# Kernel tuning notes

Measured on AMD Instinct MI355X. Metric: run time of the kernel, lower is better.

The kernel has to match this reference:

```python
import jax, jax.numpy as jnp
import numpy as np
from jax import lax

B, T, U, H, V = 4, 256, 48, 512, 1024
BLANK = V - 1  # blank = vocab_size - 1, as in Transducer.__init__


def setup_inputs() -> dict:
    key = jax.random.key(0)
    k1, k2, k3, k4 = jax.random.split(key, 4)
    enc_state = jax.random.normal(k1, (B, T, H), jnp.float32)       # encoder output
    dec_state = jax.random.normal(k2, (B, U + 1, H), jnp.float32)   # decoder output (blank-prepended targets)
    W = jax.random.normal(k3, (V, H), jnp.float32) / np.sqrt(H)     # joint proj weight
    b = jnp.zeros((V,), jnp.float32)                                # joint proj bias
    targets = jax.random.randint(k4, (B, U), 0, V - 1).astype(jnp.int32)  # labels, never blank
    inputs_length = jnp.full((B,), T, jnp.int32)
    targets_length = jnp.full((B,), U, jnp.int32)
    return {"enc_state": enc_state, "dec_state": dec_state, "W": W, "b": b,
            "targets": targets, "inputs_length": inputs_length,
            "targets_length": targets_length}


def _rnnt_loss_single(log_probs, targets, t_len, u_len):
    # log_probs: (T, U+1, V); forward-variable alpha DP of RNNT loss.
    lp_blank = log_probs[:, :, BLANK]                                   # (T, U+1)
    lp_label = jnp.take_along_axis(log_probs[:, :-1, :],
                                   targets[None, :, None], axis=2)[..., 0]  # (T, U)
    # first row: only label emissions, alpha[0,u] = sum_{k<u} lp_label[0,k]
    row0 = jnp.concatenate([jnp.zeros((1,), log_probs.dtype),
                            jnp.cumsum(lp_label[0])])                   # (U+1,)

    def row_step(prev_row, t):
        # alpha[t,u] = logaddexp(alpha[t-1,u] + blank[t-1,u], alpha[t,u-1] + label[t,u-1])
        a = prev_row + lp_blank[t - 1]                                  # (U+1,) blank transitions

        def u_step(carry, xs):
            a_u, lab = xs
            cur = jnp.logaddexp(a_u, carry + lab)
            return cur, cur

        _, rest = lax.scan(u_step, a[0], (a[1:], lp_label[t]))
        row = jnp.concatenate([a[:1], rest])
        return row, row

    _, rows = lax.scan(row_step, row0, jnp.arange(1, T))
    alpha = jnp.concatenate([row0[None], rows], axis=0)                 # (T, U+1)
    # negative log-likelihood: final blank emission from (t_len-1, u_len)
    return -(alpha[t_len - 1, u_len] + lp_blank[t_len - 1, u_len])


def reference(enc_state, dec_state, W, b, targets, inputs_length, targets_length):
    # JointNet: broadcast-add (repeat in torch) then linear projection
    joint = enc_state[:, :, None, :] + dec_state[:, None, :, :]         # (B, T, U+1, H)
    logits = jnp.einsum('btuh,vh->btuv', joint, W) + b                  # (B, T, U+1, V)
    log_probs = jax.nn.log_softmax(logits, axis=-1)
    loss = jax.vmap(_rnnt_loss_single)(log_probs, targets, inputs_length, targets_length)
    return loss  # per-sample losses (reduction='None')
```

## Files before the change

### kernel.cpp

```cpp
#include <hip/hip_runtime.h>
#include <math.h>

#define B_ 4
#define T_ 256
#define U_ 48
#define H_ 512
#define V_ 1024
#define BLANK_ (V_-1)

#define GM 1220
#define GM_ENC 1024
#define APAD 1280

#define INVLN2 1.4426950408889634f
#define LN2F   0.6931471805599453f

typedef __attribute__((ext_vector_type(8))) short short8;
typedef __attribute__((ext_vector_type(4))) float f32x4;

__device__ __forceinline__ unsigned short f2bf(float x) {
    union { float f; unsigned int u; } c; c.f = x;
    unsigned int r = c.u + 0x7FFF + ((c.u >> 16) & 1);
    return (unsigned short)(r >> 16);
}
__device__ __forceinline__ float bf2f(unsigned short u) {
    union { unsigned int i; float f; } c; c.i = ((unsigned int)u) << 16; return c.f;
}
__device__ __forceinline__ unsigned int cvt_pk_bf16(float lo, float hi) {
    unsigned int r;
    asm("v_cvt_pk_bf16_f32 %0, %1, %2" : "=v"(r) : "v"(lo), "v"(hi));
    return r;
}
__device__ __forceinline__ int wave_shr1_i(int x, int fill) {
    return __builtin_amdgcn_update_dpp(fill, x, 0x138 , 0xf, 0xf, false);
}
__device__ __forceinline__ float wave_shr1_f(float x, float fill) {
    return __builtin_bit_cast(float,
        wave_shr1_i(__builtin_bit_cast(int, x), __builtin_bit_cast(int, fill)));
}
__device__ __forceinline__ double wave_shr1_d(double x, double fill) {
    unsigned long long xb = __builtin_bit_cast(unsigned long long, x);
    unsigned long long fb = __builtin_bit_cast(unsigned long long, fill);
    int lo = wave_shr1_i((int)(unsigned)xb, (int)(unsigned)fb);
    int hi = wave_shr1_i((int)(xb >> 32), (int)(fb >> 32));
    unsigned long long r = ((unsigned long long)(unsigned)hi << 32) | (unsigned)lo;
    return __builtin_bit_cast(double, r);
}

__global__ __launch_bounds__(512) void gemm1_kernel(
    const float* __restrict__ enc, const float* __restrict__ dec,
    const float* __restrict__ W, const float* __restrict__ bias,
    unsigned short* __restrict__ Pexp)
{
    __shared__ __attribute__((aligned(16))) unsigned short As[128 * 64];
    __shared__ __attribute__((aligned(16))) unsigned short Bs[128 * 64];
    const int tid  = threadIdx.x;
    const int lane = tid & 63, wave = tid >> 6;
    const int wm = wave >> 2, wn = wave & 3;
    const int row0 = blockIdx.y * 128, col0 = blockIdx.x * 128;
    const int srow = tid >> 2;
    const int scg  = (tid & 3) * 16;

    f32x4 acc[4][2];
    #pragma unroll
    for (int mi = 0; mi < 4; ++mi)
        #pragma unroll
        for (int ni = 0; ni < 2; ++ni)
            acc[mi][ni] = (f32x4){0.f, 0.f, 0.f, 0.f};

    float4 ra[4], rb[4];
    auto loadAB = [&](int k0) {
        float4 z = make_float4(0.f, 0.f, 0.f, 0.f);
        ra[0] = ra[1] = ra[2] = ra[3] = z;
        int gr = row0 + srow;
        if (gr < GM) {
            const float* s = (gr < GM_ENC)
                ? enc + (size_t)gr * H_ + k0 + scg
                : dec + (size_t)(gr - GM_ENC) * H_ + k0 + scg;
            ra[0] = *(const float4*)s;       ra[1] = *(const float4*)(s + 4);
            ra[2] = *(const float4*)(s + 8); ra[3] = *(const float4*)(s + 12);
        }
        const float* s = W + (size_t)(col0 + srow) * H_ + k0 + scg;
        rb[0] = *(const float4*)s;       rb[1] = *(const float4*)(s + 4);
        rb[2] = *(const float4*)(s + 8); rb[3] = *(const float4*)(s + 12);
    };
    auto stage = [&]() {
        uint4 w0 = { cvt_pk_bf16(ra[0].x, ra[0].y), cvt_pk_bf16(ra[0].z, ra[0].w),
                     cvt_pk_bf16(ra[1].x, ra[1].y), cvt_pk_bf16(ra[1].z, ra[1].w) };
        uint4 w1 = { cvt_pk_bf16(ra[2].x, ra[2].y), cvt_pk_bf16(ra[2].z, ra[2].w),
                     cvt_pk_bf16(ra[3].x, ra[3].y), cvt_pk_bf16(ra[3].z, ra[3].w) };
        uint4 v0 = { cvt_pk_bf16(rb[0].x, rb[0].y), cvt_pk_bf16(rb[0].z, rb[0].w),
                     cvt_pk_bf16(rb[1].x, rb[1].y), cvt_pk_bf16(rb[1].z, rb[1].w) };
        uint4 v1 = { cvt_pk_bf16(rb[2].x, rb[2].y), cvt_pk_bf16(rb[2].z, rb[2].w),
                     cvt_pk_bf16(rb[3].x, rb[3].y), cvt_pk_bf16(rb[3].z, rb[3].w) };
        int colb = scg * 2;
        int sw0 = (colb)      ^ ((srow & 7) << 4);
        int sw1 = (colb + 16) ^ ((srow & 7) << 4);
        *(uint4*)((char*)As + srow * 128 + sw0) = w0;
        *(uint4*)((char*)As + srow * 128 + sw1) = w1;
        *(uint4*)((char*)Bs + srow * 128 + sw0) = v0;
        *(uint4*)((char*)Bs + srow * 128 + sw1) = v1;
    };
    auto compute = [&]() {
        #pragma unroll
        for (int kk = 0; kk < 2; ++kk) {
            short8 a[4], bfr[2];
            const int cb = kk * 64 + (lane >> 4) * 16;
            #pragma unroll
            for (int mi = 0; mi < 4; ++mi) {
                int r = wm * 64 + mi * 16 + (lane & 15);
                a[mi] = *(const short8*)((const char*)As + r * 128 + (cb ^ ((r & 7) << 4)));
            }
            #pragma unroll
            for (int ni = 0; ni < 2; ++ni) {
                int r = wn * 32 + ni * 16 + (lane & 15);
                bfr[ni] = *(const short8*)((const char*)Bs + r * 128 + (cb ^ ((r & 7) << 4)));
            }
            #pragma unroll
            for (int mi = 0; mi < 4; ++mi)
                #pragma unroll
                for (int ni = 0; ni < 2; ++ni)
                    asm("v_mfma_f32_16x16x32_bf16 %0, %1, %2, %0"
                        : "+v"(acc[mi][ni]) : "v"(a[mi]), "v"(bfr[ni]));
        }
    };

    loadAB(0);
    for (int k0 = 0; k0 < H_; k0 += 64) {
        stage();
        asm volatile("s_waitcnt lgkmcnt(0)" ::: "memory");
        __builtin_amdgcn_s_barrier();
        asm volatile("" ::: "memory");
        if (k0 + 64 < H_) loadAB(k0 + 64);
        compute();
        asm volatile("" ::: "memory");
        __builtin_amdgcn_s_barrier();
        asm volatile("" ::: "memory");
    }

    #pragma unroll
    for (int ni = 0; ni < 2; ++ni) {
        int col = col0 + wn * 32 + ni * 16 + (lane & 15);
        float bb = bias[col];
        #pragma unroll
        for (int mi = 0; mi < 4; ++mi) {
            #pragma unroll
            for (int j = 0; j < 4; ++j) {
                int gr = row0 + wm * 64 + mi * 16 + (lane >> 4) * 4 + j;
                if (gr >= GM) continue;
                float v = acc[mi][ni][j] + (gr < GM_ENC ? bb : 0.f);
                Pexp[(size_t)gr * V_ + col] = f2bf(__builtin_amdgcn_exp2f(v * INVLN2));
            }
        }
    }
}

__global__ __launch_bounds__(256) void gemm2_kernel(
    const unsigned short* __restrict__ Pexp, const int* __restrict__ targets,
    float* __restrict__ lp)
{
    __shared__ __attribute__((aligned(16))) unsigned short As[64 * 64];
    __shared__ __attribute__((aligned(16))) unsigned short Bs[64 * 64];
    __shared__ float eb[64];
    __shared__ float db[64];
    __shared__ float dg[64];
    __shared__ int   tgts[64];
    const int tid  = threadIdx.x;
    const int lane = tid & 63, wave = tid >> 6;
    const int wm = wave >> 1, wn = wave & 1;
    const int mt = blockIdx.x, b = blockIdx.y;

    if (tid < 64) {
        eb[tid] = bf2f(Pexp[(size_t)(b * 256 + mt * 64 + tid) * V_ + BLANK_]);
    } else if (tid < 128) {
        int u = tid - 64;
        if (u <= U_) {
            size_t drow = (size_t)(GM_ENC + b * (U_ + 1) + u);
            db[u] = bf2f(Pexp[drow * V_ + BLANK_]);
            if (u < U_) {
                int tg = targets[b * U_ + u];
                tgts[u] = tg;
                dg[u] = bf2f(Pexp[drow * V_ + tg]);
            }
        }
    }

    f32x4 acc[2][2];
    #pragma unroll
    for (int mi = 0; mi < 2; ++mi)
        #pragma unroll
        for (int ni = 0; ni < 2; ++ni)
            acc[mi][ni] = (f32x4){0.f, 0.f, 0.f, 0.f};

    short8 a2[2], b2[2];
    auto loadT = [&](int k0) {
        #pragma unroll
        for (int c = 0; c < 2; ++c) {
            int off = (tid + 256 * c) * 16;
            int row = off >> 7, colb = off & 127;
            size_t arow = (size_t)(b * 256 + mt * 64 + row);
            a2[c] = *(const short8*)((const char*)Pexp + arow * (V_*2) + k0*2 + colb);
            size_t brow = (size_t)(GM_ENC + b * (U_ + 1) + (row <= U_ ? row : U_));
            b2[c] = *(const short8*)((const char*)Pexp + brow * (V_*2) + k0*2 + colb);
        }
    };
    auto stageT = [&]() {
        #pragma unroll
        for (int c = 0; c < 2; ++c) {
            int off = (tid + 256 * c) * 16;
            int row = off >> 7, colb = off & 127;
            int sw = colb ^ ((row & 7) << 4);
            *(short8*)((char*)As + row * 128 + sw) = a2[c];
            *(short8*)((char*)Bs + row * 128 + sw) = b2[c];
        }
    };

    loadT(0);
    for (int k0 = 0; k0 < V_; k0 += 64) {
        stageT();
        asm volatile("s_waitcnt lgkmcnt(0)" ::: "memory");
        __builtin_amdgcn_s_barrier();
        asm volatile("" ::: "memory");
        if (k0 + 64 < V_) loadT(k0 + 64);
        #pragma unroll
        for (int kk = 0; kk < 2; ++kk) {
            short8 a[2], bfr[2];
            const int cb = kk * 64 + (lane >> 4) * 16;
            #pragma unroll
            for (int mi = 0; mi < 2; ++mi) {
                int r = wm * 32 + mi * 16 + (lane & 15);
                a[mi] = *(const short8*)((const char*)As + r * 128 + (cb ^ ((r & 7) << 4)));
            }
            #pragma unroll
            for (int ni = 0; ni < 2; ++ni) {
                int r = wn * 32 + ni * 16 + (lane & 15);
                bfr[ni] = *(const short8*)((const char*)Bs + r * 128 + (cb ^ ((r & 7) << 4)));
            }
            #pragma unroll
            for (int mi = 0; mi < 2; ++mi)
                #pragma unroll
                for (int ni = 0; ni < 2; ++ni)
                    asm("v_mfma_f32_16x16x32_bf16 %0, %1, %2, %0"
                        : "+v"(acc[mi][ni]) : "v"(a[mi]), "v"(bfr[ni]));
        }
        asm volatile("" ::: "memory");
        __builtin_amdgcn_s_barrier();
        asm volatile("" ::: "memory");
    }

    #pragma unroll
    for (int ni = 0; ni < 2; ++ni) {
        int u = wn * 32 + ni * 16 + (lane & 15);
        if (u > U_) continue;
        float dbu = db[u];
        float dgu = (u < U_) ? dg[u] : 0.f;
        int   tgu = (u < U_) ? tgts[u] : 0;
        #pragma unroll
        for (int mi = 0; mi < 2; ++mi) {
            #pragma unroll
            for (int j = 0; j < 4; ++j) {
                int tp = wm * 32 + mi * 16 + (lane >> 4) * 4 + j;
                int t  = mt * 64 + tp;
                float rd = __builtin_amdgcn_rcpf(acc[mi][ni][j]);
                lp[((size_t)b * 97 + u) * T_ + t] = eb[tp] * dbu * rd;
                if (u < U_) {
                    float eg = bf2f(Pexp[(size_t)(b * 256 + t) * V_ + tgu]);
                    lp[((size_t)b * 97 + 49 + u) * T_ + t] = eg * dgu * rd;
                }
            }
        }
    }
}

__global__ __launch_bounds__(256) void dp_kernel(
    const float* __restrict__ lp,
    const int* __restrict__ tlen, const int* __restrict__ ulen,
    float* __restrict__ out)
{
    __shared__ __attribute__((aligned(16))) float sm[97 * T_];
    const int b = blockIdx.x;
    const int tid = threadIdx.x;
    {
        const float4* g = (const float4*)(lp + (size_t)b * 97 * T_);
        float4* s4 = (float4*)sm;
        for (int i = tid; i < 97 * T_ / 4; i += 256) s4[i] = g[i];
    }
    __syncthreads();
    if (tid >= 64) return;

    const int l = tid;
    const int t0 = 4 * l;
    const int TL = tlen[b], UL = ulen[b];
    const int lt = (TL - 1) >> 2;
    const int smax = lt + UL;

    const int bLo = t0 * 4, bHi = t0 * 4 + U_ * 1024;
    const int lLo = 49 * 1024 + t0 * 4;
    const int lHi = 49 * 1024 + (U_ - 1) * 1024 + t0 * 4;
    int wb = -l * 1024 + t0 * 4;

    double M0 = 0.0, M1 = 0.0, M2 = 0.0, M3 = 0.0;
    int E = 0;
    float wprev = 0.f;

    float4 bqA, lqA, bqB, lqB;
    auto issue = [&](float4& bq, float4& lq) {
        int ab = min(max(wb, bLo), bHi);
        int al = min(max(wb + 48 * 1024, lLo), lHi);
        bq = *(const float4*)((const char*)sm + ab);
        lq = *(const float4*)((const char*)sm + al);
        wb += 1024;
    };
    auto step = [&](int s, const float4& bq, const float4& lq) {
        double bm = wave_shr1_d(M3, 0.0);
        int    bE = wave_shr1_i(E, 0);
        float B0f = wave_shr1_f(wprev, 0.f);
        wprev = bq.w;
        int u = s - l;
        if (u >= 0 && u <= U_) {
            int Eu = (u == 0) ? bE : E;
            double sb = ldexp(bm, bE - Eu);
            double q0 = M0 * (double)lq.x, q1 = M1 * (double)lq.y;
            double q2 = M2 * (double)lq.z, q3 = M3 * (double)lq.w;
            double A0 = fma(sb, (double)B0f, q0);
            if (s == 0 && l == 0) A0 = 1.0;
            double A1 = fma(A0, (double)bq.x, q1);
            double A2 = fma(A1, (double)bq.y, q2);
            double A3 = fma(A2, (double)bq.z, q3);
            M0 = A0; M1 = A1; M2 = A2; M3 = A3; E = Eu;
            if ((s & 7) == 7 && A3 > 0.0) {
                unsigned long long bits = __builtin_bit_cast(unsigned long long, A3);
                int e3 = (int)((bits >> 52) & 0x7FF) - 1022;
                M3 = __builtin_bit_cast(double,
                        (bits & 0x800FFFFFFFFFFFFFULL) | 0x3FE0000000000000ULL);
                M0 = ldexp(A0, -e3);
                M1 = ldexp(A1, -e3);
                M2 = ldexp(A2, -e3);
                E += e3;
            }
        }
    };

    issue(bqA, lqA);
    issue(bqB, lqB);
    int s = 0;
    for (; s + 1 <= smax; s += 2) {
        step(s, bqA, lqA);     issue(bqA, lqA);
        step(s + 1, bqB, lqB); issue(bqB, lqB);
    }
    if (s <= smax) step(s, bqA, lqA);

    if (l == lt) {
        int j = (TL - 1) & 3;
        double rm = (j == 0) ? M0 : (j == 1) ? M1 : (j == 2) ? M2 : M3;
        unsigned long long rb = __builtin_bit_cast(unsigned long long, rm);
        int re = (int)((rb >> 52) & 0x7FF) - 1022;
        double rmn = __builtin_bit_cast(double,
                       (rb & 0x800FFFFFFFFFFFFFULL) | 0x3FE0000000000000ULL);
        float lfin = __builtin_amdgcn_logf((float)rmn) + (float)(re + E)
                   + __builtin_amdgcn_logf(sm[UL * T_ + (TL - 1)]);
        out[b] = -lfin * LN2F;
    }
}

extern "C" void kernel_launch(void* const* d_in, const int* in_sizes, int n_in,
                              void* d_out, int out_size, void* d_ws, size_t ws_size,
                              hipStream_t stream) {
    const float* enc     = (const float*)d_in[0];
    const float* dec     = (const float*)d_in[1];
    const float* W       = (const float*)d_in[2];
    const float* bias    = (const float*)d_in[3];
    const int*   targets = (const int*)d_in[4];
    const int*   tlen    = (const int*)d_in[5];
    const int*   ulen    = (const int*)d_in[6];
    float* out = (float*)d_out;

    unsigned short* Pexp = (unsigned short*)d_ws;
    float* lp = (float*)(Pexp + (size_t)APAD * V_);

    gemm1_kernel<<<dim3(V_/128, APAD/128), dim3(512), 0, stream>>>(
        enc, dec, W, bias, Pexp);

    gemm2_kernel<<<dim3(4, B_), dim3(256), 0, stream>>>(Pexp, targets, lp);

    dp_kernel<<<dim3(B_), dim3(256), 0, stream>>>(lp, tlen, ulen, out);
}
```

Measured before the change: 57.04 us.

## Load full-K tiles into LDS once in gemm1 with smaller 64x64 tiles

The gemm1 kernel moves from 128x128 tiles with a pipelined K loop of 64 to 64x64 tiles. Each block now stages the whole K=512 slice of A and B into LDS (64 KB per operand) in one pass, behind a single barrier, then runs 16 MFMA steps with no further synchronization. The grid grows from 80 to 320 blocks to fill more CUs, at the cost of 128 KB of LDS per block (limiting occupancy to about one block per CU), less operand reuse, and no overlap between global loads and MFMA work.

```diff
diff --git a/kernel.cpp b/kernel.cpp
--- a/kernel.cpp
+++ b/kernel.cpp
@@ -47,95 +47,71 @@
     return __builtin_bit_cast(double, r);
 }
 
-__global__ __launch_bounds__(512) void gemm1_kernel(
+__global__ __launch_bounds__(256) void gemm1_kernel(
     const float* __restrict__ enc, const float* __restrict__ dec,
     const float* __restrict__ W, const float* __restrict__ bias,
     unsigned short* __restrict__ Pexp)
 {
-    __shared__ __attribute__((aligned(16))) unsigned short As[128 * 64];
-    __shared__ __attribute__((aligned(16))) unsigned short Bs[128 * 64];
+    __shared__ __attribute__((aligned(16))) unsigned short As[64 * 512];
+    __shared__ __attribute__((aligned(16))) unsigned short Bs[64 * 512];
     const int tid  = threadIdx.x;
     const int lane = tid & 63, wave = tid >> 6;
-    const int wm = wave >> 2, wn = wave & 3;
-    const int row0 = blockIdx.y * 128, col0 = blockIdx.x * 128;
+    const int wm = wave >> 1, wn = wave & 1;
+    const int row0 = blockIdx.y * 64, col0 = blockIdx.x * 64;
     const int srow = tid >> 2;
-    const int scg  = (tid & 3) * 16;
-
-    f32x4 acc[4][2];
-    #pragma unroll
-    for (int mi = 0; mi < 4; ++mi)
+    const int c0   = (tid & 3) * 128;
+
+    {
+        int gr = row0 + srow;
+        const float* sa = (gr < GM_ENC) ? enc + (size_t)gr * H_
+                        : (gr < GM)     ? dec + (size_t)(gr - GM_ENC) * H_
+                                        : (const float*)0;
+        const float* sw_ = W + (size_t)(col0 + srow) * H_;
+        #pragma unroll
+        for (int j = 0; j < 16; ++j) {
+            int ce  = c0 + j * 8;
+            int byt = srow * 1024 + ((ce * 2) ^ ((srow & 7) << 4));
+            float4 x0 = make_float4(0.f,0.f,0.f,0.f), x1 = x0;
+            if (sa) { x0 = *(const float4*)(sa + ce); x1 = *(const float4*)(sa + ce + 4); }
+            uint4 wa = { cvt_pk_bf16(x0.x,x0.y), cvt_pk_bf16(x0.z,x0.w),
+                         cvt_pk_bf16(x1.x,x1.y), cvt_pk_bf16(x1.z,x1.w) };
+            *(uint4*)((char*)As + byt) = wa;
+            float4 y0 = *(const float4*)(sw_ + ce);
+            float4 y1 = *(const float4*)(sw_ + ce + 4);
+            uint4 wb = { cvt_pk_bf16(y0.x,y0.y), cvt_pk_bf16(y0.z,y0.w),
+                         cvt_pk_bf16(y1.x,y1.y), cvt_pk_bf16(y1.z,y1.w) };
+            *(uint4*)((char*)Bs + byt) = wb;
+        }
+    }
+    __syncthreads();
+
+    f32x4 acc[2][2];
+    #pragma unroll
+    for (int mi = 0; mi < 2; ++mi)
         #pragma unroll
         for (int ni = 0; ni < 2; ++ni)
             acc[mi][ni] = (f32x4){0.f, 0.f, 0.f, 0.f};
 
-    float4 ra[4], rb[4];
-    auto loadAB = [&](int k0) {
-        float4 z = make_float4(0.f, 0.f, 0.f, 0.f);
-        ra[0] = ra[1] = ra[2] = ra[3] = z;
-        int gr = row0 + srow;
-        if (gr < GM) {
-            const float* s = (gr < GM_ENC)
-                ? enc + (size_t)gr * H_ + k0 + scg
-                : dec + (size_t)(gr - GM_ENC) * H_ + k0 + scg;
-            ra[0] = *(const float4*)s;       ra[1] = *(const float4*)(s + 4);
-            ra[2] = *(const float4*)(s + 8); ra[3] = *(const float4*)(s + 12);
-        }
-        const float* s = W + (size_t)(col0 + srow) * H_ + k0 + scg;
-        rb[0] = *(const float4*)s;       rb[1] = *(const float4*)(s + 4);
-        rb[2] = *(const float4*)(s + 8); rb[3] = *(const float4*)(s + 12);
-    };
-    auto stage = [&]() {
-        uint4 w0 = { cvt_pk_bf16(ra[0].x, ra[0].y), cvt_pk_bf16(ra[0].z, ra[0].w),
-                     cvt_pk_bf16(ra[1].x, ra[1].y), cvt_pk_bf16(ra[1].z, ra[1].w) };
-        uint4 w1 = { cvt_pk_bf16(ra[2].x, ra[2].y), cvt_pk_bf16(ra[2].z, ra[2].w),
-                     cvt_pk_bf16(ra[3].x, ra[3].y), cvt_pk_bf16(ra[3].z, ra[3].w) };
-        uint4 v0 = { cvt_pk_bf16(rb[0].x, rb[0].y), cvt_pk_bf16(rb[0].z, rb[0].w),
-                     cvt_pk_bf16(rb[1].x, rb[1].y), cvt_pk_bf16(rb[1].z, rb[1].w) };
-        uint4 v1 = { cvt_pk_bf16(rb[2].x, rb[2].y), cvt_pk_bf16(rb[2].z, rb[2].w),
-                     cvt_pk_bf16(rb[3].x, rb[3].y), cvt_pk_bf16(rb[3].z, rb[3].w) };
-        int colb = scg * 2;
-        int sw0 = (colb)      ^ ((srow & 7) << 4);
-        int sw1 = (colb + 16) ^ ((srow & 7) << 4);
-        *(uint4*)((char*)As + srow * 128 + sw0) = w0;
-        *(uint4*)((char*)As + srow * 128 + sw1) = w1;
-        *(uint4*)((char*)Bs + srow * 128 + sw0) = v0;
-        *(uint4*)((char*)Bs + srow * 128 + sw1) = v1;
-    };
-    auto compute = [&]() {
-        #pragma unroll
-        for (int kk = 0; kk < 2; ++kk) {
-            short8 a[4], bfr[2];
-            const int cb = kk * 64 + (lane >> 4) * 16;
-            #pragma unroll
-            for (int mi = 0; mi < 4; ++mi) {
-                int r = wm * 64 + mi * 16 + (lane & 15);
-                a[mi] = *(const short8*)((const char*)As + r * 128 + (cb ^ ((r & 7) << 4)));
-            }
-            #pragma unroll
-            for (int ni = 0; ni < 2; ++ni) {
-                int r = wn * 32 + ni * 16 + (lane & 15);
-                bfr[ni] = *(const short8*)((const char*)Bs + r * 128 + (cb ^ ((r & 7) << 4)));
-            }
-            #pragma unroll
-            for (int mi = 0; mi < 4; ++mi)
-                #pragma unroll
-                for (int ni = 0; ni < 2; ++ni)
-                    asm("v_mfma_f32_16x16x32_bf16 %0, %1, %2, %0"
-                        : "+v"(acc[mi][ni]) : "v"(a[mi]), "v"(bfr[ni]));
-        }
-    };
-
-    loadAB(0);
-    for (int k0 = 0; k0 < H_; k0 += 64) {
-        stage();
-        asm volatile("s_waitcnt lgkmcnt(0)" ::: "memory");
-        __builtin_amdgcn_s_barrier();
-        asm volatile("" ::: "memory");
-        if (k0 + 64 < H_) loadAB(k0 + 64);
-        compute();
-        asm volatile("" ::: "memory");
-        __builtin_amdgcn_s_barrier();
-        asm volatile("" ::: "memory");
+    #pragma unroll
+    for (int kk = 0; kk < 16; ++kk) {
+        short8 a[2], b[2];
+        const int cb = kk * 64 + (lane >> 4) * 16;
+        #pragma unroll
+        for (int mi = 0; mi < 2; ++mi) {
+            int r = wm * 32 + mi * 16 + (lane & 15);
+            a[mi] = *(const short8*)((const char*)As + r * 1024 + (cb ^ ((r & 7) << 4)));
+        }
+        #pragma unroll
+        for (int ni = 0; ni < 2; ++ni) {
+            int r = wn * 32 + ni * 16 + (lane & 15);
+            b[ni] = *(const short8*)((const char*)Bs + r * 1024 + (cb ^ ((r & 7) << 4)));
+        }
+        #pragma unroll
+        for (int mi = 0; mi < 2; ++mi)
+            #pragma unroll
+            for (int ni = 0; ni < 2; ++ni)
+                asm("v_mfma_f32_16x16x32_bf16 %0, %1, %2, %0"
+                    : "+v"(acc[mi][ni]) : "v"(a[mi]), "v"(b[ni]));
     }
 
     #pragma unroll
@@ -143,10 +119,10 @@
         int col = col0 + wn * 32 + ni * 16 + (lane & 15);
         float bb = bias[col];
         #pragma unroll
-        for (int mi = 0; mi < 4; ++mi) {
+        for (int mi = 0; mi < 2; ++mi) {
             #pragma unroll
             for (int j = 0; j < 4; ++j) {
-                int gr = row0 + wm * 64 + mi * 16 + (lane >> 4) * 4 + j;
+                int gr = row0 + wm * 32 + mi * 16 + (lane >> 4) * 4 + j;
                 if (gr >= GM) continue;
                 float v = acc[mi][ni][j] + (gr < GM_ENC ? bb : 0.f);
                 Pexp[(size_t)gr * V_ + col] = f2bf(__builtin_amdgcn_exp2f(v * INVLN2));
@@ -378,7 +354,7 @@
     unsigned short* Pexp = (unsigned short*)d_ws;
     float* lp = (float*)(Pexp + (size_t)APAD * V_);
 
-    gemm1_kernel<<<dim3(V_/128, APAD/128), dim3(512), 0, stream>>>(
+    gemm1_kernel<<<dim3(V_/64, APAD/64), dim3(256), 0, stream>>>(
         enc, dec, W, bias, Pexp);
 
     gemm2_kernel<<<dim3(4, B_), dim3(256), 0, stream>>>(Pexp, targets, lp);
```

New measurement: 61.58 us. +8.0%, slower.
